# Performance work log

Measured on AMD Instinct MI355X. Metric: run time of the kernel, lower is better.

The kernel has to match this reference:

```python
import jax, jax.numpy as jnp
import numpy as np


def setup_inputs() -> dict:
    key = jax.random.key(0)
    ks = jax.random.split(key, 4)
    B, T, D, U = 32, 1024, 1024, 1024
    x = jax.random.normal(ks[0], (B, T, D), dtype=jnp.float32)
    W = jax.random.normal(ks[1], (D, 4 * U), dtype=jnp.float32) * (1.0 / np.sqrt(D))
    b = jnp.zeros((4 * U,), dtype=jnp.float32)
    Vr = jax.random.normal(ks[2], (U,), dtype=jnp.float32) * 0.1
    Vf = jax.random.normal(ks[3], (U,), dtype=jnp.float32) * 0.1
    h0 = jnp.zeros((B, U), dtype=jnp.float32)
    c0 = jnp.zeros((B, U), dtype=jnp.float32)
    return {"x": x, "h0": h0, "c0": c0, "W": W, "b": b, "Vr": Vr, "Vf": Vf}


def _sru(x, h0, c0, W, b, Vr, Vf):
    B, T, D = x.shape
    U = Vr.shape[0]
    # Batched matmul across all timesteps, then sequential elementwise scan.
    g = jnp.einsum('btd,dk->btk', x, W) + b            # [B, T, 4U]
    g = jnp.moveaxis(g, 1, 0)                          # [T, B, 4U]
    g1, g2, g3, g4 = jnp.split(g, 4, axis=-1)          # each [T, B, U]

    def step(c_, gs):
        a1, a2, a3, a4 = gs
        f = jax.nn.sigmoid(a1 + Vf * c_)
        c = f * c_ + (1.0 - f) * a2
        r = jax.nn.sigmoid(a3 + Vr * c_)
        h = r * c + (1.0 - r) * a4
        return c, h

    c_last, hs = jax.lax.scan(step, c0, (g1, g2, g3, g4))
    return jnp.moveaxis(hs, 0, 1)                      # [B, T, U]


def reference(x, h0, c0, W, b, Vr, Vf):
    return _sru(x, h0, c0, W, b, Vr, Vf)
```

## Files before the change

kernel.cpp:

```cpp
#include <hip/hip_runtime.h>
#include <cstdint>
#include <cstddef>

typedef short short8 __attribute__((ext_vector_type(8)));
typedef short s16x4 __attribute__((ext_vector_type(4)));
typedef float f32x4 __attribute__((ext_vector_type(4)));

typedef const __attribute__((address_space(1))) void* gas_ptr;
typedef __attribute__((address_space(3))) void* las_ptr;

__device__ __forceinline__ unsigned short f2bf(float f) {
    unsigned int u = __float_as_uint(f);
    u += 0x7fffu + ((u >> 16) & 1u);
    return (unsigned short)(u >> 16);
}
__device__ __forceinline__ float bf2f(unsigned short s) {
    return __uint_as_float(((unsigned int)s) << 16);
}
__device__ __forceinline__ float sigmoid_f(float z) {
    return __builtin_amdgcn_rcpf(1.0f + __expf(-z));
}
__device__ __forceinline__ void async_copy16(const void* gp, void* lp) {
    __builtin_amdgcn_global_load_lds((gas_ptr)gp, (las_ptr)lp, 16, 0, 0);
}

__global__ __launch_bounds__(256) void cvt_x_kernel(const float* __restrict__ in,
                                                    unsigned short* __restrict__ out) {
    size_t i = ((size_t)blockIdx.x * 256 + threadIdx.x) * 8;
    float4 v0 = *(const float4*)(in + i);
    float4 v1 = *(const float4*)(in + i + 4);
    short8 o;
    o[0]=(short)f2bf(v0.x); o[1]=(short)f2bf(v0.y); o[2]=(short)f2bf(v0.z); o[3]=(short)f2bf(v0.w);
    o[4]=(short)f2bf(v1.x); o[5]=(short)f2bf(v1.y); o[6]=(short)f2bf(v1.z); o[7]=(short)f2bf(v1.w);
    *(short8*)(out + i) = o;
}

__global__ __launch_bounds__(256) void cvt_w_kernel(const float* __restrict__ W,
                                                    unsigned short* __restrict__ Wt) {
    __shared__ unsigned short tile[64][65];
    int bk = blockIdx.x >> 6, bn = blockIdx.x & 63;
    int k0 = bk * 64, n0 = bn * 64;
    int t = threadIdx.x;
    int cr = t >> 6;
    int cc = t & 63;
#pragma unroll
    for (int i = 0; i < 16; ++i) {
        int row = i * 4 + cr;
        tile[row][cc] = f2bf(W[(size_t)(k0 + row) * 4096 + n0 + cc]);
    }
    __syncthreads();
#pragma unroll
    for (int i = 0; i < 16; ++i) {
        int nrow = i * 4 + cr;
        Wt[(size_t)(n0 + nrow) * 1024 + k0 + cc] = tile[cc][nrow];
    }
}

__global__ __launch_bounds__(256, 2) void gemm_kernel(const unsigned short* __restrict__ A,
                                                      const unsigned short* __restrict__ Bt,
                                                      const float* __restrict__ bias,
                                                      unsigned short* __restrict__ gT) {
    __shared__ __align__(16) unsigned short As[128 * 64];
    __shared__ __align__(16) unsigned short Bs[128 * 64];

    int bid = blockIdx.x;
    int band = bid >> 8;
    int r = bid & 255;
    int mt = band * 8 + (r >> 5);
    int nt = r & 31;
    int m0 = mt * 128, n0 = nt * 128;

    int tidx = threadIdx.x;
    int lane = tidx & 63, wv = tidx >> 6;
    int wm = wv >> 1, wn = wv & 1;
    int l15 = lane & 15, quad = lane >> 4;

    f32x4 acc[4][4] = {};

    for (int k0 = 0; k0 < 1024; k0 += 64) {
        __syncthreads();
#pragma unroll
        for (int i = 0; i < 4; ++i) {
            int ci = (wv * 4 + i) * 64 + lane;
            int row = ci >> 3, cc = ci & 7;
            int sc = (cc ^ (row & 7)) << 3;
            const unsigned short* ga = A + (size_t)(m0 + row) * 1024 + k0 + sc;
            async_copy16(ga, (char*)As + (wv * 4 + i) * 1024);
            const unsigned short* gb = Bt + (size_t)(n0 + row) * 1024 + k0 + sc;
            async_copy16(gb, (char*)Bs + (wv * 4 + i) * 1024);
        }
        __syncthreads();
#pragma unroll
        for (int kt = 0; kt < 2; ++kt) {
            short8 af[4], bf[4];
#pragma unroll
            for (int mt2 = 0; mt2 < 4; ++mt2) {
                int row = wm * 64 + mt2 * 16 + l15;
                int kc = kt * 4 + quad;
                af[mt2] = *(const short8*)((const char*)As + row * 128 + ((kc ^ (row & 7)) << 4));
            }
#pragma unroll
            for (int nt2 = 0; nt2 < 4; ++nt2) {
                int rown = wn * 64 + nt2 * 16 + l15;
                int kc = kt * 4 + quad;
                bf[nt2] = *(const short8*)((const char*)Bs + rown * 128 + ((kc ^ (rown & 7)) << 4));
            }
#pragma unroll
            for (int mt2 = 0; mt2 < 4; ++mt2)
#pragma unroll
                for (int nt2 = 0; nt2 < 4; ++nt2)
                    acc[mt2][nt2] = __builtin_amdgcn_mfma_f32_16x16x32_bf16(
                        af[mt2], bf[nt2], acc[mt2][nt2], 0, 0, 0);
        }
    }

#pragma unroll
    for (int mt2 = 0; mt2 < 4; ++mt2) {
        int mbase = m0 + wm * 64 + mt2 * 16 + quad * 4;
        int b_ = mbase >> 10, t_ = mbase & 1023;
#pragma unroll
        for (int nt2 = 0; nt2 < 4; ++nt2) {
            int n = n0 + wn * 64 + nt2 * 16 + l15;
            int gate = n >> 10, u = n & 1023;
            float bv = bias[n];
            s16x4 pk;
            pk[0] = (short)f2bf(acc[mt2][nt2][0] + bv);
            pk[1] = (short)f2bf(acc[mt2][nt2][1] + bv);
            pk[2] = (short)f2bf(acc[mt2][nt2][2] + bv);
            pk[3] = (short)f2bf(acc[mt2][nt2][3] + bv);
            size_t off = ((((size_t)(t_ >> 3) * 32 + (size_t)b_) * 4 + (size_t)gate) << 13)
                         + ((size_t)u << 3) + (size_t)(t_ & 7);
            *(s16x4*)(gT + off) = pk;
        }
    }
}

__global__ __launch_bounds__(512) void scan_c_kernel(const unsigned short* __restrict__ gT,
                                                     const float* __restrict__ c0,
                                                     const float* __restrict__ Vf,
                                                     float* __restrict__ cB) {
    __shared__ __align__(16) unsigned short sbuf[2 * 2 * 16 * 512];

    const int NCH = 7;
    int blk = blockIdx.x;
    int b = blk >> 4;
    int u0 = (blk & 15) << 6;
    int tid = threadIdx.x;
    int wv = tid >> 6;
    int lane = tid & 63;

    size_t gbase = (size_t)b * 32768 + ((size_t)(u0 + lane) << 3);

    if (wv >= 1) {
        for (int p = wv - 1; p < 32; p += 7) {
            int gate = p >> 4, tbi = p & 15;
            const unsigned short* src = gT + (((size_t)tbi) << 20) + gbase + gate * 8192;
            char* dst = (char*)sbuf + gate * 16384 + tbi * 1024 + lane * 16;
            async_copy16(src, dst);
        }
    }
    __syncthreads();

    float c = 0.0f, vf = 0.0f;
    if (wv == 0) {
        int u = u0 + lane;
        c = c0[(b << 10) + u];
        vf = Vf[u];
    }

    for (int k = 0; k < NCH; ++k) {
        if (wv >= 1) {
            if (k + 1 < NCH) {
                int nb = (k + 1) & 1;
                for (int p = wv - 1; p < 32; p += 7) {
                    int gate = p >> 4, tbi = p & 15;
                    const unsigned short* src =
                        gT + (((size_t)((k + 1) * 16 + tbi)) << 20) + gbase + gate * 8192;
                    char* dst = (char*)sbuf + nb * 32768 + gate * 16384 + tbi * 1024 + lane * 16;
                    async_copy16(src, dst);
                }
            }
        } else {
            const unsigned short* ls = sbuf + (k & 1) * 16384 + (size_t)lane * 8;
#pragma unroll
            for (int tbi = 0; tbi < 16; ++tbi) {
                short8 a1 = *(const short8*)(ls + tbi * 512);
                short8 a2 = *(const short8*)(ls + 8192 + tbi * 512);
#pragma unroll
                for (int i = 0; i < 8; ++i) {
                    float x1 = bf2f((unsigned short)a1[i]);
                    float x2 = bf2f((unsigned short)a2[i]);
                    float f  = sigmoid_f(x1 + vf * c);
                    c = fmaf(f, c - x2, x2);
                }
            }
            cB[((size_t)k << 15) + (size_t)(b << 10) + (size_t)(u0 + lane)] = c;
        }
        __syncthreads();
    }
}

__global__ __launch_bounds__(256) void scan_h_kernel(const unsigned short* __restrict__ gT,
                                                     const float* __restrict__ c0,
                                                     const float* __restrict__ cB,
                                                     const float* __restrict__ Vr,
                                                     const float* __restrict__ Vf,
                                                     float* __restrict__ h) {
    int idx = blockIdx.x * 256 + threadIdx.x;
    int u = idx & 1023;
    int rb = idx >> 10;
    int r = rb >> 5, b = rb & 31;
    float vf = Vf[u], vr = Vr[u];
    float c = (r == 0) ? c0[(b << 10) + u]
                       : cB[((size_t)(r - 1) << 15) + (size_t)(b << 10) + u];
    const unsigned short* base = gT + ((size_t)b * 4) * 8192 + ((size_t)u << 3);
    float* hb = h + ((size_t)b << 20) + u;
    int tb0 = r << 4;

    const unsigned short* p0 = base + ((size_t)tb0 << 20);
    short8 n1 = *(const short8*)(p0);
    short8 n2 = *(const short8*)(p0 + 8192);
    short8 n3 = *(const short8*)(p0 + 16384);
    short8 n4 = *(const short8*)(p0 + 24576);
    for (int j = 0; j < 16; ++j) {
        short8 a1 = n1, a2 = n2, a3 = n3, a4 = n4;
        if (j < 15) {
            const unsigned short* q = base + ((size_t)(tb0 + j + 1) << 20);
            n1 = *(const short8*)(q);
            n2 = *(const short8*)(q + 8192);
            n3 = *(const short8*)(q + 16384);
            n4 = *(const short8*)(q + 24576);
        }
        int t0 = (tb0 + j) * 8;
#pragma unroll
        for (int i = 0; i < 8; ++i) {
            float x1 = bf2f((unsigned short)a1[i]);
            float x2 = bf2f((unsigned short)a2[i]);
            float x3 = bf2f((unsigned short)a3[i]);
            float x4 = bf2f((unsigned short)a4[i]);
            float f  = sigmoid_f(x1 + vf * c);
            float cp = c;
            c = fmaf(f, c - x2, x2);
            float rr = sigmoid_f(x3 + vr * cp);
            float hv = fmaf(rr, c - x4, x4);
            hb[(size_t)(t0 + i) << 10] = hv;
        }
    }
}

extern "C" void kernel_launch(void* const* d_in, const int* in_sizes, int n_in,
                              void* d_out, int out_size, void* d_ws, size_t ws_size,
                              hipStream_t stream) {
    const float* x  = (const float*)d_in[0];
    const float* c0 = (const float*)d_in[2];
    const float* W  = (const float*)d_in[3];
    const float* b  = (const float*)d_in[4];
    const float* Vr = (const float*)d_in[5];
    const float* Vf = (const float*)d_in[6];
    float* h = (float*)d_out;

    char* ws = (char*)d_ws;
    unsigned short* xb = (unsigned short*)ws;
    unsigned short* wt = (unsigned short*)(ws + (size_t)67108864);
    unsigned short* gT = (unsigned short*)(ws + (size_t)75497472);
    float* cB = (float*)ws;

    cvt_x_kernel<<<16384, 256, 0, stream>>>(x, xb);
    cvt_w_kernel<<<1024, 256, 0, stream>>>(W, wt);
    gemm_kernel<<<8192, 256, 0, stream>>>(xb, wt, b, gT);
    scan_c_kernel<<<512, 512, 0, stream>>>(gT, c0, Vf, cB);
    scan_h_kernel<<<1024, 256, 0, stream>>>(gT, c0, cB, Vr, Vf, h);
}
```

Measured before the change: 579.4 us.

## Fuse two-pass chunked scan into a single sequential scan kernel

Replaces the two-phase scheme with one kernel that runs the whole 1024-step recurrence per (batch, unit) lane. The old scheme first computed chunk-boundary cell states and then recomputed h in 8 parallel time segments; the new kernel computes c and h together and writes h directly. Its async LDS double-buffer now stages all four gates in 8-time-block chunks. This removes one kernel launch, the cB round trip and the second read of the gate tensor. In exchange, h production loses the 8-way time parallelism and the single serial compute wave per block now also does the reset-gate sigmoid and the h stores.

```diff
diff --git a/kernel.cpp b/kernel.cpp
--- a/kernel.cpp
+++ b/kernel.cpp
@@ -135,13 +135,14 @@
     }
 }
 
-__global__ __launch_bounds__(512) void scan_c_kernel(const unsigned short* __restrict__ gT,
-                                                     const float* __restrict__ c0,
-                                                     const float* __restrict__ Vf,
-                                                     float* __restrict__ cB) {
-    __shared__ __align__(16) unsigned short sbuf[2 * 2 * 16 * 512];
-
-    const int NCH = 7;
+__global__ __launch_bounds__(512, 4) void scan_kernel(const unsigned short* __restrict__ gT,
+                                                      const float* __restrict__ c0,
+                                                      const float* __restrict__ Vr,
+                                                      const float* __restrict__ Vf,
+                                                      float* __restrict__ h) {
+    __shared__ __align__(16) unsigned short sbuf[2 * 4 * 8 * 512];
+
+    const int NCH = 16;
     int blk = blockIdx.x;
     int b = blk >> 4;
     int u0 = (blk & 15) << 6;
@@ -153,19 +154,22 @@
 
     if (wv >= 1) {
         for (int p = wv - 1; p < 32; p += 7) {
-            int gate = p >> 4, tbi = p & 15;
-            const unsigned short* src = gT + (((size_t)tbi) << 20) + gbase + gate * 8192;
-            char* dst = (char*)sbuf + gate * 16384 + tbi * 1024 + lane * 16;
+            int gate = p >> 3, tbi = p & 7;
+            const unsigned short* src = gT + ((size_t)tbi << 20) + gbase + gate * 8192;
+            char* dst = (char*)sbuf + gate * 8192 + tbi * 1024 + lane * 16;
             async_copy16(src, dst);
         }
     }
     __syncthreads();
 
-    float c = 0.0f, vf = 0.0f;
+    float c = 0.0f, vf = 0.0f, vr = 0.0f;
+    float* hb = nullptr;
     if (wv == 0) {
         int u = u0 + lane;
         c = c0[(b << 10) + u];
         vf = Vf[u];
+        vr = Vr[u];
+        hb = h + ((size_t)b << 20) + u;
     }
 
     for (int k = 0; k < NCH; ++k) {
@@ -173,78 +177,38 @@
             if (k + 1 < NCH) {
                 int nb = (k + 1) & 1;
                 for (int p = wv - 1; p < 32; p += 7) {
-                    int gate = p >> 4, tbi = p & 15;
+                    int gate = p >> 3, tbi = p & 7;
                     const unsigned short* src =
-                        gT + (((size_t)((k + 1) * 16 + tbi)) << 20) + gbase + gate * 8192;
-                    char* dst = (char*)sbuf + nb * 32768 + gate * 16384 + tbi * 1024 + lane * 16;
+                        gT + ((size_t)((k + 1) * 8 + tbi) << 20) + gbase + gate * 8192;
+                    char* dst = (char*)sbuf + nb * 32768 + gate * 8192 + tbi * 1024 + lane * 16;
                     async_copy16(src, dst);
                 }
             }
         } else {
             const unsigned short* ls = sbuf + (k & 1) * 16384 + (size_t)lane * 8;
 #pragma unroll
-            for (int tbi = 0; tbi < 16; ++tbi) {
+            for (int tbi = 0; tbi < 8; ++tbi) {
                 short8 a1 = *(const short8*)(ls + tbi * 512);
-                short8 a2 = *(const short8*)(ls + 8192 + tbi * 512);
+                short8 a2 = *(const short8*)(ls + 4096 + tbi * 512);
+                short8 a3 = *(const short8*)(ls + 8192 + tbi * 512);
+                short8 a4 = *(const short8*)(ls + 12288 + tbi * 512);
+                int t0 = (k * 8 + tbi) * 8;
 #pragma unroll
                 for (int i = 0; i < 8; ++i) {
                     float x1 = bf2f((unsigned short)a1[i]);
                     float x2 = bf2f((unsigned short)a2[i]);
+                    float x3 = bf2f((unsigned short)a3[i]);
+                    float x4 = bf2f((unsigned short)a4[i]);
                     float f  = sigmoid_f(x1 + vf * c);
+                    float cp = c;
                     c = fmaf(f, c - x2, x2);
+                    float rr = sigmoid_f(x3 + vr * cp);
+                    float hv = fmaf(rr, c - x4, x4);
+                    hb[(size_t)(t0 + i) << 10] = hv;
                 }
             }
-            cB[((size_t)k << 15) + (size_t)(b << 10) + (size_t)(u0 + lane)] = c;
         }
         __syncthreads();
-    }
-}
-
-__global__ __launch_bounds__(256) void scan_h_kernel(const unsigned short* __restrict__ gT,
-                                                     const float* __restrict__ c0,
-                                                     const float* __restrict__ cB,
-                                                     const float* __restrict__ Vr,
-                                                     const float* __restrict__ Vf,
-                                                     float* __restrict__ h) {
-    int idx = blockIdx.x * 256 + threadIdx.x;
-    int u = idx & 1023;
-    int rb = idx >> 10;
-    int r = rb >> 5, b = rb & 31;
-    float vf = Vf[u], vr = Vr[u];
-    float c = (r == 0) ? c0[(b << 10) + u]
-                       : cB[((size_t)(r - 1) << 15) + (size_t)(b << 10) + u];
-    const unsigned short* base = gT + ((size_t)b * 4) * 8192 + ((size_t)u << 3);
-    float* hb = h + ((size_t)b << 20) + u;
-    int tb0 = r << 4;
-
-    const unsigned short* p0 = base + ((size_t)tb0 << 20);
-    short8 n1 = *(const short8*)(p0);
-    short8 n2 = *(const short8*)(p0 + 8192);
-    short8 n3 = *(const short8*)(p0 + 16384);
-    short8 n4 = *(const short8*)(p0 + 24576);
-    for (int j = 0; j < 16; ++j) {
-        short8 a1 = n1, a2 = n2, a3 = n3, a4 = n4;
-        if (j < 15) {
-            const unsigned short* q = base + ((size_t)(tb0 + j + 1) << 20);
-            n1 = *(const short8*)(q);
-            n2 = *(const short8*)(q + 8192);
-            n3 = *(const short8*)(q + 16384);
-            n4 = *(const short8*)(q + 24576);
-        }
-        int t0 = (tb0 + j) * 8;
-#pragma unroll
-        for (int i = 0; i < 8; ++i) {
-            float x1 = bf2f((unsigned short)a1[i]);
-            float x2 = bf2f((unsigned short)a2[i]);
-            float x3 = bf2f((unsigned short)a3[i]);
-            float x4 = bf2f((unsigned short)a4[i]);
-            float f  = sigmoid_f(x1 + vf * c);
-            float cp = c;
-            c = fmaf(f, c - x2, x2);
-            float rr = sigmoid_f(x3 + vr * cp);
-            float hv = fmaf(rr, c - x4, x4);
-            hb[(size_t)(t0 + i) << 10] = hv;
-        }
     }
 }
 
@@ -263,11 +227,9 @@
     unsigned short* xb = (unsigned short*)ws;
     unsigned short* wt = (unsigned short*)(ws + (size_t)67108864);
     unsigned short* gT = (unsigned short*)(ws + (size_t)75497472);
-    float* cB = (float*)ws;
 
     cvt_x_kernel<<<16384, 256, 0, stream>>>(x, xb);
     cvt_w_kernel<<<1024, 256, 0, stream>>>(W, wt);
     gemm_kernel<<<8192, 256, 0, stream>>>(xb, wt, b, gT);
-    scan_c_kernel<<<512, 512, 0, stream>>>(gT, c0, Vf, cB);
-    scan_h_kernel<<<1024, 256, 0, stream>>>(gT, c0, cB, Vr, Vf, h);
-}
+    scan_kernel<<<512, 512, 0, stream>>>(gT, c0, Vr, Vf, h);
+}
```

Result: faster. 562.6 us (-2.9%).
